# Kernel optimization log

Measured on AMD Instinct MI355X. Metric: run time of the kernel, lower is better.

The kernel has to match this reference:

```python
import jax, jax.numpy as jnp
import numpy as np

N_EDGES = 320000
N_PARTICLES = 10000
EMBED = 256
N_RBF = 16
OUT_EMBED = 512


def setup_inputs() -> dict:
    key = jax.random.key(0)
    ks = jax.random.split(key, 9)
    s = 0.05
    return {
        "messages": jax.random.normal(ks[0], (N_EDGES, EMBED), dtype=jnp.float32),
        "rbf": jax.random.normal(ks[1], (N_EDGES, N_RBF), dtype=jnp.float32),
        "idx_i": jax.random.randint(ks[2], (N_EDGES,), 0, N_PARTICLES, dtype=jnp.int32),
        "W_rbf": jax.random.normal(ks[3], (N_RBF, EMBED), dtype=jnp.float32) * s,
        "W_up": jax.random.normal(ks[4], (EMBED, OUT_EMBED), dtype=jnp.float32) * s,
        "W_d0": jax.random.normal(ks[5], (OUT_EMBED, OUT_EMBED), dtype=jnp.float32) * s,
        "b_d0": jnp.zeros((OUT_EMBED,), dtype=jnp.float32),
        "W_d1": jax.random.normal(ks[6], (OUT_EMBED, OUT_EMBED), dtype=jnp.float32) * s,
        "b_d1": jnp.zeros((OUT_EMBED,), dtype=jnp.float32),
        "W_final": jax.random.normal(ks[7], (OUT_EMBED, 1), dtype=jnp.float32) * s,
    }


def reference(messages, rbf, idx_i, W_rbf, W_up, W_d0, b_d0, W_d1, b_d1, W_final):
    # rbf_dense: [n_edges, n_rbf] @ [n_rbf, embed] -> gate per edge
    transformed_rbf = rbf @ W_rbf
    gated = messages * transformed_rbf                      # [n_edges, embed]
    # high-precision scatter-add over receiver atoms (fp32 accumulation)
    summed = jax.ops.segment_sum(gated, idx_i, num_segments=N_PARTICLES)
    up = summed @ W_up                                      # [n_particles, out_embed]
    up = jax.nn.swish(up @ W_d0 + b_d0)
    up = jax.nn.swish(up @ W_d1 + b_d1)
    per_atom_targets = up @ W_final                         # [n_particles, 1]
    return per_atom_targets
```

## Files before the change

### kernel.cpp

```cpp
#include <hip/hip_runtime.h>
#include <hip/hip_bf16.h>
#include <math.h>

#define N_EDGES_C 320000
#define N_PART 10000
#define EMBED 256
#define NRBF 16
#define OUTE 512

typedef __attribute__((ext_vector_type(8))) short short8;
typedef __attribute__((ext_vector_type(4))) float float4v;

#define WS_SUMMED   0
#define WS_BUF0     6000000
#define WS_BUF1     17000000
#define WS_WTUP     28000000
#define WS_WTD0     28300000
#define WS_WTD1     28900000
#define WS_CNT      29500000
#define WS_CUR      29540000
#define WS_OFF      29580000
#define WS_ELIST    29640000

__global__ __launch_bounds__(256) void hist_kernel(
    const int* __restrict__ idx_i, int* __restrict__ cnt)
{
    int e = blockIdx.x * 256 + threadIdx.x;
    if (e < N_EDGES_C) atomicAdd(&cnt[idx_i[e]], 1);
}

__global__ __launch_bounds__(1024) void scan_kernel(
    const int* __restrict__ cnt, int* __restrict__ off)
{
    __shared__ int s[1024];
    const int t = threadIdx.x;
    const int base = t * 10;
    int v[10];
    int loc = 0;
#pragma unroll
    for (int i = 0; i < 10; ++i) {
        int idx = base + i;
        int c = (idx < N_PART) ? cnt[idx] : 0;
        v[i] = c;
        loc += c;
    }
    s[t] = loc;
    __syncthreads();
    for (int d = 1; d < 1024; d <<= 1) {
        int x = (t >= d) ? s[t - d] : 0;
        __syncthreads();
        s[t] += x;
        __syncthreads();
    }
    int pre = (t > 0) ? s[t - 1] : 0;
#pragma unroll
    for (int i = 0; i < 10; ++i) {
        int idx = base + i;
        if (idx < N_PART) off[idx] = pre;
        pre += v[i];
    }
}

__global__ __launch_bounds__(256) void fill_kernel(
    const int* __restrict__ idx_i, const int* __restrict__ off,
    int* __restrict__ cur, int* __restrict__ elist)
{
    int e = blockIdx.x * 256 + threadIdx.x;
    if (e >= N_EDGES_C) return;
    int p = idx_i[e];
    int pos = atomicAdd(&cur[p], 1);
    elist[off[p] + pos] = e;
}

__device__ __forceinline__ float rbf_gate(
    const float* __restrict__ rbf, int e, const float (*w)[EMBED], int c)
{
    const float4* r4 = (const float4*)(rbf + (size_t)e * NRBF);
    float4 r0 = r4[0], r1 = r4[1], r2 = r4[2], r3 = r4[3];
    float t = 0.f;
    t = fmaf(r0.x, w[0][c], t);  t = fmaf(r0.y, w[1][c], t);
    t = fmaf(r0.z, w[2][c], t);  t = fmaf(r0.w, w[3][c], t);
    t = fmaf(r1.x, w[4][c], t);  t = fmaf(r1.y, w[5][c], t);
    t = fmaf(r1.z, w[6][c], t);  t = fmaf(r1.w, w[7][c], t);
    t = fmaf(r2.x, w[8][c], t);  t = fmaf(r2.y, w[9][c], t);
    t = fmaf(r2.z, w[10][c], t); t = fmaf(r2.w, w[11][c], t);
    t = fmaf(r3.x, w[12][c], t); t = fmaf(r3.y, w[13][c], t);
    t = fmaf(r3.z, w[14][c], t); t = fmaf(r3.w, w[15][c], t);
    return t;
}

__global__ __launch_bounds__(256) void gather_kernel(
    const float* __restrict__ messages, const float* __restrict__ rbf,
    const float* __restrict__ W_rbf, const int* __restrict__ off,
    const int* __restrict__ cnt, const int* __restrict__ elist,
    __hip_bfloat16* __restrict__ summed)
{
    __shared__ float w[NRBF][EMBED];
    __shared__ int el[256];
    const int c = threadIdx.x;
    const int p = blockIdx.x;
#pragma unroll
    for (int k = 0; k < NRBF; ++k) w[k][c] = W_rbf[k * EMBED + c];

    const int base = off[p];
    const int deg  = cnt[p];
    float acc = 0.f;

    for (int ch = 0; ch < deg; ch += 256) {
        const int n = min(256, deg - ch);
        if (c < n) el[c] = elist[base + ch + c];
        __syncthreads();

        int j = 0;
        for (; j + 4 <= n; j += 4) {
            const int e0 = el[j], e1 = el[j + 1], e2 = el[j + 2], e3 = el[j + 3];
            const float m0 = messages[(size_t)e0 * EMBED + c];
            const float m1 = messages[(size_t)e1 * EMBED + c];
            const float m2 = messages[(size_t)e2 * EMBED + c];
            const float m3 = messages[(size_t)e3 * EMBED + c];
            const float t0 = rbf_gate(rbf, e0, w, c);
            const float t1 = rbf_gate(rbf, e1, w, c);
            const float t2 = rbf_gate(rbf, e2, w, c);
            const float t3 = rbf_gate(rbf, e3, w, c);
            acc = fmaf(m0, t0, acc);
            acc = fmaf(m1, t1, acc);
            acc = fmaf(m2, t2, acc);
            acc = fmaf(m3, t3, acc);
        }
        for (; j < n; ++j) {
            const int e = el[j];
            const float m = messages[(size_t)e * EMBED + c];
            acc = fmaf(m, rbf_gate(rbf, e, w, c), acc);
        }
        __syncthreads();
    }
    summed[(size_t)p * EMBED + c] = __float2bfloat16(acc);
}

__global__ __launch_bounds__(256) void transpose_cvt_all(
    const float* __restrict__ W_up, const float* __restrict__ W_d0,
    const float* __restrict__ W_d1, __hip_bfloat16* __restrict__ wt_up,
    __hip_bfloat16* __restrict__ wt_d0, __hip_bfloat16* __restrict__ wt_d1)
{
    const int z = blockIdx.z;
    const float* W = (z == 0) ? W_up : (z == 1) ? W_d0 : W_d1;
    __hip_bfloat16* Wt = (z == 0) ? wt_up : (z == 1) ? wt_d0 : wt_d1;
    const int K = (z == 0) ? EMBED : OUTE;
    const int N = OUTE;
    if (blockIdx.y * 32 >= K) return;

    __shared__ float t[32][33];
    const int bn = blockIdx.x * 32;
    const int bk = blockIdx.y * 32;
    const int x = threadIdx.x & 31;
    const int y8 = threadIdx.x >> 5;
#pragma unroll
    for (int yy = y8; yy < 32; yy += 8)
        t[yy][x] = W[(size_t)(bk + yy) * N + bn + x];
    __syncthreads();
#pragma unroll
    for (int yy = y8; yy < 32; yy += 8)
        Wt[(size_t)(bn + yy) * K + bk + x] = __float2bfloat16(t[x][yy]);
}

#define BM 128
#define BN 128
#define BK 32
#define LDSP 40

template <int ACT, int FUSE>
__global__ __launch_bounds__(256) void gemm_mfma(
    const __hip_bfloat16* __restrict__ A,
    const __hip_bfloat16* __restrict__ Bt,
    const float* __restrict__ bias,
    __hip_bfloat16* __restrict__ C,
    const float* __restrict__ Wf,
    float* __restrict__ out,
    int M, int K, int N)
{
    __shared__ short As[BM * LDSP];
    __shared__ short Bs[BN * LDSP];

    const int tid  = threadIdx.x;
    const int bm   = blockIdx.x * BM;
    const int bn   = blockIdx.y * BN;
    const int wave = tid >> 6;
    const int lane = tid & 63;
    const int wm   = (wave >> 1) * 64;
    const int wn   = (wave & 1) * 64;
    const int l16  = lane & 15;
    const int quad = lane >> 4;

    float4v acc[4][4];
#pragma unroll
    for (int i = 0; i < 4; ++i)
#pragma unroll
        for (int j = 0; j < 4; ++j)
#pragma unroll
            for (int r = 0; r < 4; ++r) acc[i][j][r] = 0.f;

    const int sr = tid >> 1;
    const int sh = (tid & 1) * 16;

    for (int k0 = 0; k0 < K; k0 += BK) {
        short8 av0, av1;
        if (bm + sr < M) {
            const short8* ga = (const short8*)((const short*)A + (size_t)(bm + sr) * K + k0 + sh);
            av0 = ga[0];
            av1 = ga[1];
        } else {
#pragma unroll
            for (int i = 0; i < 8; ++i) { av0[i] = 0; av1[i] = 0; }
        }
        *(short8*)&As[sr * LDSP + sh]     = av0;
        *(short8*)&As[sr * LDSP + sh + 8] = av1;
        const short8* gb = (const short8*)((const short*)Bt + (size_t)(bn + sr) * K + k0 + sh);
        short8 bv0 = gb[0], bv1 = gb[1];
        *(short8*)&Bs[sr * LDSP + sh]     = bv0;
        *(short8*)&Bs[sr * LDSP + sh + 8] = bv1;
        __syncthreads();

        short8 af[4], bf[4];
#pragma unroll
        for (int mt = 0; mt < 4; ++mt)
            af[mt] = *(const short8*)&As[(wm + mt * 16 + l16) * LDSP + quad * 8];
#pragma unroll
        for (int nt = 0; nt < 4; ++nt)
            bf[nt] = *(const short8*)&Bs[(wn + nt * 16 + l16) * LDSP + quad * 8];
#pragma unroll
        for (int mt = 0; mt < 4; ++mt)
#pragma unroll
            for (int nt = 0; nt < 4; ++nt)
                acc[mt][nt] = __builtin_amdgcn_mfma_f32_16x16x32_bf16(
                    af[mt], bf[nt], acc[mt][nt], 0, 0, 0);
        __syncthreads();
    }

    if (!FUSE) {
#pragma unroll
        for (int mt = 0; mt < 4; ++mt) {
            const int row0 = bm + wm + mt * 16 + quad * 4;
#pragma unroll
            for (int nt = 0; nt < 4; ++nt) {
                const int col = bn + wn + nt * 16 + l16;
                const float bv = bias ? bias[col] : 0.f;
#pragma unroll
                for (int r = 0; r < 4; ++r) {
                    const int rr = row0 + r;
                    if (rr < M) {
                        float v = acc[mt][nt][r] + bv;
                        if (ACT == 1) v = v / (1.f + expf(-v));
                        C[(size_t)rr * N + col] = __float2bfloat16(v);
                    }
                }
            }
        }
    } else {
        float bv[4], wfv[4];
#pragma unroll
        for (int nt = 0; nt < 4; ++nt) {
            const int col = bn + wn + nt * 16 + l16;
            bv[nt]  = bias ? bias[col] : 0.f;
            wfv[nt] = Wf[col];
        }
#pragma unroll
        for (int mt = 0; mt < 4; ++mt) {
#pragma unroll
            for (int r = 0; r < 4; ++r) {
                const int row = bm + wm + mt * 16 + quad * 4 + r;
                float s = 0.f;
#pragma unroll
                for (int nt = 0; nt < 4; ++nt) {
                    float v = acc[mt][nt][r] + bv[nt];
                    if (ACT == 1) v = v / (1.f + expf(-v));
                    s = fmaf(v, wfv[nt], s);
                }
#pragma unroll
                for (int o = 8; o > 0; o >>= 1) s += __shfl_down(s, o);
                if (l16 == 0 && row < M) atomicAdd(&out[row], s);
            }
        }
    }
}

extern "C" void kernel_launch(void* const* d_in, const int* in_sizes, int n_in,
                              void* d_out, int out_size, void* d_ws, size_t ws_size,
                              hipStream_t stream) {
    const float* messages = (const float*)d_in[0];
    const float* rbf      = (const float*)d_in[1];
    const int*   idx_i    = (const int*)d_in[2];
    const float* W_rbf    = (const float*)d_in[3];
    const float* W_up     = (const float*)d_in[4];
    const float* W_d0     = (const float*)d_in[5];
    const float* b_d0     = (const float*)d_in[6];
    const float* W_d1     = (const float*)d_in[7];
    const float* b_d1     = (const float*)d_in[8];
    const float* W_final  = (const float*)d_in[9];
    float* out = (float*)d_out;

    char* ws = (char*)d_ws;
    __hip_bfloat16* summed = (__hip_bfloat16*)(ws + WS_SUMMED);
    __hip_bfloat16* buf0   = (__hip_bfloat16*)(ws + WS_BUF0);
    __hip_bfloat16* buf1   = (__hip_bfloat16*)(ws + WS_BUF1);
    __hip_bfloat16* wt_up  = (__hip_bfloat16*)(ws + WS_WTUP);
    __hip_bfloat16* wt_d0  = (__hip_bfloat16*)(ws + WS_WTD0);
    __hip_bfloat16* wt_d1  = (__hip_bfloat16*)(ws + WS_WTD1);
    int* cnt   = (int*)(ws + WS_CNT);
    int* cur   = (int*)(ws + WS_CUR);
    int* offp  = (int*)(ws + WS_OFF);
    int* elist = (int*)(ws + WS_ELIST);

    hipMemsetAsync(ws + WS_CNT, 0, 80000, stream);
    hipMemsetAsync(d_out, 0, (size_t)N_PART * sizeof(float), stream);

    hist_kernel<<<(N_EDGES_C + 255) / 256, 256, 0, stream>>>(idx_i, cnt);
    scan_kernel<<<1, 1024, 0, stream>>>(cnt, offp);
    fill_kernel<<<(N_EDGES_C + 255) / 256, 256, 0, stream>>>(idx_i, offp, cur, elist);

    transpose_cvt_all<<<dim3(OUTE / 32, OUTE / 32, 3), 256, 0, stream>>>(
        W_up, W_d0, W_d1, wt_up, wt_d0, wt_d1);

    gather_kernel<<<N_PART, 256, 0, stream>>>(messages, rbf, W_rbf, offp, cnt,
                                              elist, summed);

    dim3 g((N_PART + BM - 1) / BM, OUTE / BN);
    gemm_mfma<0, 0><<<g, 256, 0, stream>>>(summed, wt_up, nullptr, buf0,
                                           nullptr, nullptr, N_PART, EMBED, OUTE);
    gemm_mfma<1, 0><<<g, 256, 0, stream>>>(buf0, wt_d0, b_d0, buf1,
                                           nullptr, nullptr, N_PART, OUTE, OUTE);
    gemm_mfma<1, 1><<<g, 256, 0, stream>>>(buf1, wt_d1, b_d1, nullptr,
                                           W_final, out, N_PART, OUTE, OUTE);
}
```

Before: 627.6 us.

## Split gather edges across waves with float4 columns and register-resident W_rbf

The gather kernel now gives each of the four waves its own strided subset of a particle's edges. Each lane handles four embedding columns with float4 loads and keeps its W_rbf slice in registers instead of shared memory. Partial sums are combined through a small shared-memory reduction, and the next edge index is prefetched. This removes the shared-memory edge-list staging and per-chunk barriers and makes message loads wider, at the cost of more registers per thread and a final cross-wave reduction.

```diff
diff --git a/kernel.cpp b/kernel.cpp
--- a/kernel.cpp
+++ b/kernel.cpp
@@ -72,69 +72,58 @@
     elist[off[p] + pos] = e;
 }
 
-__device__ __forceinline__ float rbf_gate(
-    const float* __restrict__ rbf, int e, const float (*w)[EMBED], int c)
-{
-    const float4* r4 = (const float4*)(rbf + (size_t)e * NRBF);
-    float4 r0 = r4[0], r1 = r4[1], r2 = r4[2], r3 = r4[3];
-    float t = 0.f;
-    t = fmaf(r0.x, w[0][c], t);  t = fmaf(r0.y, w[1][c], t);
-    t = fmaf(r0.z, w[2][c], t);  t = fmaf(r0.w, w[3][c], t);
-    t = fmaf(r1.x, w[4][c], t);  t = fmaf(r1.y, w[5][c], t);
-    t = fmaf(r1.z, w[6][c], t);  t = fmaf(r1.w, w[7][c], t);
-    t = fmaf(r2.x, w[8][c], t);  t = fmaf(r2.y, w[9][c], t);
-    t = fmaf(r2.z, w[10][c], t); t = fmaf(r2.w, w[11][c], t);
-    t = fmaf(r3.x, w[12][c], t); t = fmaf(r3.y, w[13][c], t);
-    t = fmaf(r3.z, w[14][c], t); t = fmaf(r3.w, w[15][c], t);
-    return t;
-}
-
 __global__ __launch_bounds__(256) void gather_kernel(
     const float* __restrict__ messages, const float* __restrict__ rbf,
     const float* __restrict__ W_rbf, const int* __restrict__ off,
     const int* __restrict__ cnt, const int* __restrict__ elist,
     __hip_bfloat16* __restrict__ summed)
 {
-    __shared__ float w[NRBF][EMBED];
-    __shared__ int el[256];
-    const int c = threadIdx.x;
-    const int p = blockIdx.x;
-#pragma unroll
-    for (int k = 0; k < NRBF; ++k) w[k][c] = W_rbf[k * EMBED + c];
+    __shared__ float red[4][EMBED];
+    const int tid  = threadIdx.x;
+    const int wave = tid >> 6;
+    const int lane = tid & 63;
+    const int c4   = lane << 2;
+    const int p    = blockIdx.x;
+
+    float4v wr[16];
+#pragma unroll
+    for (int k = 0; k < 16; ++k)
+        wr[k] = *(const float4v*)(W_rbf + k * EMBED + c4);
 
     const int base = off[p];
     const int deg  = cnt[p];
-    float acc = 0.f;
-
-    for (int ch = 0; ch < deg; ch += 256) {
-        const int n = min(256, deg - ch);
-        if (c < n) el[c] = elist[base + ch + c];
-        __syncthreads();
-
-        int j = 0;
-        for (; j + 4 <= n; j += 4) {
-            const int e0 = el[j], e1 = el[j + 1], e2 = el[j + 2], e3 = el[j + 3];
-            const float m0 = messages[(size_t)e0 * EMBED + c];
-            const float m1 = messages[(size_t)e1 * EMBED + c];
-            const float m2 = messages[(size_t)e2 * EMBED + c];
-            const float m3 = messages[(size_t)e3 * EMBED + c];
-            const float t0 = rbf_gate(rbf, e0, w, c);
-            const float t1 = rbf_gate(rbf, e1, w, c);
-            const float t2 = rbf_gate(rbf, e2, w, c);
-            const float t3 = rbf_gate(rbf, e3, w, c);
-            acc = fmaf(m0, t0, acc);
-            acc = fmaf(m1, t1, acc);
-            acc = fmaf(m2, t2, acc);
-            acc = fmaf(m3, t3, acc);
-        }
-        for (; j < n; ++j) {
-            const int e = el[j];
-            const float m = messages[(size_t)e * EMBED + c];
-            acc = fmaf(m, rbf_gate(rbf, e, w, c), acc);
-        }
-        __syncthreads();
-    }
-    summed[(size_t)p * EMBED + c] = __float2bfloat16(acc);
+
+    float4v acc = {0.f, 0.f, 0.f, 0.f};
+
+    int j = wave;
+    int e_next = (j < deg) ? elist[base + j] : 0;
+    for (; j < deg; j += 4) {
+        const int e = e_next;
+        if (j + 4 < deg) e_next = elist[base + j + 4];
+        const float4v* r4 = (const float4v*)(rbf + (size_t)e * NRBF);
+        const float4v r0 = r4[0], r1 = r4[1], r2 = r4[2], r3 = r4[3];
+        const float4v m  = *(const float4v*)(messages + (size_t)e * EMBED + c4);
+        float4v t = {0.f, 0.f, 0.f, 0.f};
+#define GATE(rv, comp, kk)                                   \
+        t[0] = fmaf(rv[comp], wr[kk][0], t[0]);              \
+        t[1] = fmaf(rv[comp], wr[kk][1], t[1]);              \
+        t[2] = fmaf(rv[comp], wr[kk][2], t[2]);              \
+        t[3] = fmaf(rv[comp], wr[kk][3], t[3]);
+        GATE(r0, 0, 0)  GATE(r0, 1, 1)  GATE(r0, 2, 2)  GATE(r0, 3, 3)
+        GATE(r1, 0, 4)  GATE(r1, 1, 5)  GATE(r1, 2, 6)  GATE(r1, 3, 7)
+        GATE(r2, 0, 8)  GATE(r2, 1, 9)  GATE(r2, 2, 10) GATE(r2, 3, 11)
+        GATE(r3, 0, 12) GATE(r3, 1, 13) GATE(r3, 2, 14) GATE(r3, 3, 15)
+#undef GATE
+        acc[0] = fmaf(m[0], t[0], acc[0]);
+        acc[1] = fmaf(m[1], t[1], acc[1]);
+        acc[2] = fmaf(m[2], t[2], acc[2]);
+        acc[3] = fmaf(m[3], t[3], acc[3]);
+    }
+
+    *(float4v*)&red[wave][c4] = acc;
+    __syncthreads();
+    const float s = red[0][tid] + red[1][tid] + red[2][tid] + red[3][tid];
+    summed[(size_t)p * EMBED + tid] = __float2bfloat16(s);
 }
 
 __global__ __launch_bounds__(256) void transpose_cvt_all(
```

New measurement: 650.8 us. +3.7%, slower.
